# Performance work log

Measured on AMD Instinct MI355X. Metric: run time of the kernel, lower is better.

The kernel has to match this reference:

```python
import jax, jax.numpy as jnp
import numpy as np

DIM = 1536
RMS_EPS = 1e-7
LN_EPS = 1e-5


def rmsnorm(x, w):
    ms = jnp.mean(x * x, axis=-1, keepdims=True)
    return x / jnp.sqrt(ms + RMS_EPS) * w


def layernorm(x, w, b):
    mu = jnp.mean(x, axis=-1, keepdims=True)
    var = jnp.mean((x - mu) ** 2, axis=-1, keepdims=True)
    return (x - mu) / jnp.sqrt(var + LN_EPS) * w + b


def linear(x, W, b):
    # W stored as (in, out)
    return jnp.einsum('bnd,df->bnf', x, W) + b


def setup_inputs() -> dict:
    key = jax.random.key(0)
    ks = jax.random.split(key, 32)
    D = DIM
    s = 0.02
    inp = {
        'x': jax.random.normal(ks[0], (2, 4096, D), jnp.float32),
        'text_emb': jax.random.normal(ks[1], (2, 512, D), jnp.float32),
        # norm params
        'sq_w': jnp.ones((D,), jnp.float32),
        'sk_w': jnp.ones((D,), jnp.float32),
        'cq_w': jnp.ones((D,), jnp.float32),
        'ck_w': jnp.ones((D,), jnp.float32),
        'ln_w': jnp.ones((D,), jnp.float32),
        'ln_b': jnp.zeros((D,), jnp.float32),
        # self-attn projections
        'Wq': jax.random.normal(ks[2], (D, D), jnp.float32) * s,
        'bq': jnp.zeros((D,), jnp.float32),
        'Wk': jax.random.normal(ks[3], (D, D), jnp.float32) * s,
        'bk': jnp.zeros((D,), jnp.float32),
        'Wv': jax.random.normal(ks[4], (D, D), jnp.float32) * s,
        'bv': jnp.zeros((D,), jnp.float32),
        'Wo': jax.random.normal(ks[5], (D, D), jnp.float32) * s,
        'bo': jnp.zeros((D,), jnp.float32),
        # cross-attn projections
        'CWq': jax.random.normal(ks[6], (D, D), jnp.float32) * s,
        'Cbq': jnp.zeros((D,), jnp.float32),
        'CWk': jax.random.normal(ks[7], (D, D), jnp.float32) * s,
        'Cbk': jnp.zeros((D,), jnp.float32),
        'CWv': jax.random.normal(ks[8], (D, D), jnp.float32) * s,
        'Cbv': jnp.zeros((D,), jnp.float32),
        'CWo': jax.random.normal(ks[9], (D, D), jnp.float32) * s,
        'Cbo': jnp.zeros((D,), jnp.float32),
        # FFN
        'W1': jax.random.normal(ks[10], (D, 4 * D), jnp.float32) * s,
        'b1': jnp.zeros((4 * D,), jnp.float32),
        'W2': jax.random.normal(ks[11], (4 * D, D), jnp.float32) * s,
        'b2': jnp.zeros((D,), jnp.float32),
    }
    return inp


def reference(x, text_emb, sq_w, sk_w, cq_w, ck_w, ln_w, ln_b,
              Wq, bq, Wk, bk, Wv, bv, Wo, bo,
              CWq, Cbq, CWk, Cbk, CWv, Cbv, CWo, Cbo,
              W1, b1, W2, b2):
    scale = 1.0 / jnp.sqrt(jnp.float32(DIM))  # NOTE: full-dim scale, no head split (faithful)

    # self-attention (single-head over full dim)
    q = linear(rmsnorm(x, sq_w), Wq, bq)
    k = linear(rmsnorm(x, sk_w), Wk, bk)
    v = linear(x, Wv, bv)
    attn = jax.nn.softmax(jnp.einsum('bnd,bmd->bnm', q, k) * scale, axis=-1)
    attn_out = linear(jnp.einsum('bnm,bmd->bnd', attn, v), Wo, bo)

    # cross-attention
    cq = linear(rmsnorm(x, cq_w), CWq, Cbq)
    ck = linear(rmsnorm(text_emb, ck_w), CWk, Cbk)
    cv = linear(text_emb, CWv, Cbv)
    cattn = jax.nn.softmax(jnp.einsum('bnd,bmd->bnm', cq, ck) * scale, axis=-1)
    cross_out = linear(jnp.einsum('bnm,bmd->bnd', cattn, cv), CWo, Cbo)

    # FFN with exact GELU (torch nn.GELU default)
    h = linear(layernorm(x, ln_w, ln_b), W1, b1)
    ffn_out = linear(jax.nn.gelu(h, approximate=False), W2, b2)

    return x + attn_out + cross_out + ffn_out
```

## Files before the change

kernel.cpp:

```cpp
#include <hip/hip_runtime.h>
#include <hip/hip_bf16.h>
#include <cmath>

#define DD 1536
#define FF 6144

typedef __bf16 bf16_t;
typedef __bf16 bf16x8 __attribute__((ext_vector_type(8)));
typedef __bf16 bf16x4 __attribute__((ext_vector_type(4)));
typedef float  f32x4  __attribute__((ext_vector_type(4)));

#define VM6 asm volatile("s_waitcnt vmcnt(6)" ::: "memory")
#define VM0 asm volatile("s_waitcnt vmcnt(0)" ::: "memory")
#define LGKM0 do { asm volatile("s_waitcnt lgkmcnt(0)" :::); __builtin_amdgcn_sched_barrier(0); } while (0)
#define BAR __builtin_amdgcn_s_barrier()

__device__ __forceinline__ void async_load16(const bf16_t* g, bf16_t* l) {
  __builtin_amdgcn_global_load_lds(
      (const __attribute__((address_space(1))) void*)g,
      (__attribute__((address_space(3))) void*)l, 16, 0, 0);
}

__device__ __forceinline__ bf16x8 ds_read128(unsigned int addr) {
  bf16x8 r;
  asm volatile("ds_read_b128 %0, %1" : "=v"(r) : "v"(addr));
  return r;
}

__device__ __forceinline__ void xcd_remap(int& bx, int& by) {
  const int gx = gridDim.x, gy = gridDim.y;
  int wg = by * gx + bx;
  const int nwg = gx * gy;
  const int q = nwg >> 3, r = nwg & 7, xcd = wg & 7, o = wg >> 3;
  wg = (xcd < r ? xcd * (q + 1) : r * (q + 1) + (xcd - r) * q) + o;
  bx = wg % gx;
  by = wg / gx;
}

__global__ __launch_bounds__(256) void transpose_to_bf16(
    const float* __restrict__ W, bf16_t* __restrict__ Wt, int K, int N,
    const float* __restrict__ s, int ldt) {
  __shared__ float tile[32][33];
  const int tx = threadIdx.x, ty = threadIdx.y;
  const int n0 = blockIdx.x * 32, k0 = blockIdx.y * 32;
#pragma unroll
  for (int i = 0; i < 4; i++)
    tile[ty + 8 * i][tx] = W[(size_t)(k0 + ty + 8 * i) * N + n0 + tx];
  __syncthreads();
  const float sc = (s != nullptr) ? s[k0 + tx] : 1.f;
#pragma unroll
  for (int i = 0; i < 4; i++)
    Wt[(size_t)(n0 + ty + 8 * i) * ldt + k0 + tx] = (bf16_t)(tile[tx][ty + 8 * i] * sc);
}

__global__ __launch_bounds__(256) void bias_add2(
    const float* __restrict__ a, const float* __restrict__ b, float* __restrict__ o, int n) {
  const int i = blockIdx.x * 256 + threadIdx.x;
  if (i < n) o[i] = a[i] + b[i];
}

__device__ __forceinline__ void breduce1(float& a) {
#pragma unroll
  for (int off = 32; off; off >>= 1) a += __shfl_xor(a, off);
  __shared__ float sa[4];
  const int w = threadIdx.x >> 6, ln = threadIdx.x & 63;
  if (ln == 0) sa[w] = a;
  __syncthreads();
  a = (sa[0] + sa[1]) + (sa[2] + sa[3]);
  __syncthreads();
}

__device__ __forceinline__ void breduce2(float& a, float& b) {
#pragma unroll
  for (int off = 32; off; off >>= 1) {
    a += __shfl_xor(a, off);
    b += __shfl_xor(b, off);
  }
  __shared__ float sa[4], sb[4];
  const int w = threadIdx.x >> 6, ln = threadIdx.x & 63;
  if (ln == 0) { sa[w] = a; sb[w] = b; }
  __syncthreads();
  a = (sa[0] + sa[1]) + (sa[2] + sa[3]);
  b = (sb[0] + sb[1]) + (sb[2] + sb[3]);
  __syncthreads();
}

__global__ __launch_bounds__(256) void norm_x2(
    const float* __restrict__ x, bf16_t* __restrict__ xr, bf16_t* __restrict__ xb) {
  const int row = blockIdx.x, t = threadIdx.x;
  const float* p = x + (size_t)row * DD;
  f32x4 v0 = ((const f32x4*)p)[t];
  f32x4 v1 = 0.0f;
  if (t < 128) v1 = ((const f32x4*)p)[256 + t];
  float s2 = 0.f;
#pragma unroll
  for (int e = 0; e < 4; e++) s2 += v0[e] * v0[e];
  if (t < 128) {
#pragma unroll
    for (int e = 0; e < 4; e++) s2 += v1[e] * v1[e];
  }
  breduce1(s2);
  const float rq = rsqrtf(s2 * (1.f / DD) + 1e-7f);
  auto emit = [&](int ci, f32x4 v) {
    bf16x4 orr, ob;
#pragma unroll
    for (int e = 0; e < 4; e++) {
      orr[e] = (bf16_t)(v[e] * rq);
      ob[e] = (bf16_t)v[e];
    }
    const size_t o = (size_t)row * DD + ci * 4;
    *(bf16x4*)(xr + o) = orr;
    *(bf16x4*)(xb + o) = ob;
  };
  emit(t, v0);
  if (t < 128) emit(256 + t, v1);
}

__global__ __launch_bounds__(256) void norm_ln(
    const float* __restrict__ x, const float* __restrict__ w,
    const float* __restrict__ bb, bf16_t* __restrict__ o) {
  const int row = blockIdx.x, t = threadIdx.x;
  const float* p = x + (size_t)row * DD;
  f32x4 v0 = ((const f32x4*)p)[t];
  f32x4 v1 = 0.0f;
  if (t < 128) v1 = ((const f32x4*)p)[256 + t];
  float s = 0.f, s2 = 0.f;
#pragma unroll
  for (int e = 0; e < 4; e++) { s += v0[e]; s2 += v0[e] * v0[e]; }
  if (t < 128) {
#pragma unroll
    for (int e = 0; e < 4; e++) { s += v1[e]; s2 += v1[e] * v1[e]; }
  }
  breduce2(s, s2);
  const float mu = s * (1.f / DD);
  const float rln = rsqrtf(s2 * (1.f / DD) - mu * mu + 1e-5f);
  auto emit = [&](int ci, f32x4 v) {
    const int i0 = ci * 4;
    bf16x4 ov;
#pragma unroll
    for (int e = 0; e < 4; e++)
      ov[e] = (bf16_t)((v[e] - mu) * rln * w[i0 + e] + bb[i0 + e]);
    *(bf16x4*)(o + (size_t)row * DD + i0) = ov;
  };
  emit(t, v0);
  if (t < 128) emit(256 + t, v1);
}

__global__ __launch_bounds__(256) void norm_t2(
    const float* __restrict__ te, bf16_t* __restrict__ tb, bf16_t* __restrict__ tck) {
  const int row = blockIdx.x, t = threadIdx.x;
  const float* p = te + (size_t)row * DD;
  f32x4 v0 = ((const f32x4*)p)[t];
  f32x4 v1 = 0.0f;
  if (t < 128) v1 = ((const f32x4*)p)[256 + t];
  float s2 = 0.f;
#pragma unroll
  for (int e = 0; e < 4; e++) s2 += v0[e] * v0[e];
  if (t < 128) {
#pragma unroll
    for (int e = 0; e < 4; e++) s2 += v1[e] * v1[e];
  }
  breduce1(s2);
  const float rq = rsqrtf(s2 * (1.f / DD) + 1e-7f);
  auto emit = [&](int ci, f32x4 v) {
    bf16x4 ob, oc;
#pragma unroll
    for (int e = 0; e < 4; e++) {
      ob[e] = (bf16_t)v[e];
      oc[e] = (bf16_t)(v[e] * rq);
    }
    const size_t o = (size_t)row * DD + ci * 4;
    *(bf16x4*)(tb + o) = ob;
    *(bf16x4*)(tck + o) = oc;
  };
  emit(t, v0);
  if (t < 128) emit(256 + t, v1);
}

template <int NC>
__global__ __launch_bounds__(256) void softmax_bf16(bf16_t* __restrict__ S) {
  const int t = threadIdx.x;
  bf16_t* sr = S + (size_t)blockIdx.x * NC;
  constexpr int NV = (NC / 8 + 255) / 256;
  float v[NV][8];
  float mx = -3.4e38f;
#pragma unroll
  for (int i = 0; i < NV; i++) {
    const int idx = t + i * 256;
    if (idx * 8 < NC) {
      bf16x8 b = ((const bf16x8*)sr)[idx];
#pragma unroll
      for (int e = 0; e < 8; e++) {
        v[i][e] = (float)b[e];
        mx = fmaxf(mx, v[i][e]);
      }
    }
  }
#pragma unroll
  for (int off = 32; off; off >>= 1) mx = fmaxf(mx, __shfl_xor(mx, off));
  __shared__ float sm[4];
  const int w = t >> 6, ln = t & 63;
  if (ln == 0) sm[w] = mx;
  __syncthreads();
  mx = fmaxf(fmaxf(sm[0], sm[1]), fmaxf(sm[2], sm[3]));
  __syncthreads();
  float sum = 0.f;
#pragma unroll
  for (int i = 0; i < NV; i++) {
    const int idx = t + i * 256;
    if (idx * 8 < NC) {
#pragma unroll
      for (int e = 0; e < 8; e++) {
        v[i][e] = __expf(v[i][e] - mx);
        sum += v[i][e];
      }
    }
  }
#pragma unroll
  for (int off = 32; off; off >>= 1) sum += __shfl_xor(sum, off);
  __shared__ float ss[4];
  if (ln == 0) ss[w] = sum;
  __syncthreads();
  sum = (ss[0] + ss[1]) + (ss[2] + ss[3]);
  const float inv = 1.f / sum;
#pragma unroll
  for (int i = 0; i < NV; i++) {
    const int idx = t + i * 256;
    if (idx * 8 < NC) {
      bf16x8 o;
#pragma unroll
      for (int e = 0; e < 8; e++) o[e] = (bf16_t)(v[i][e] * inv);
      ((bf16x8*)sr)[idx] = o;
    }
  }
}

enum { EPI_BF16 = 0, EPI_F32_SCALE = 1, EPI_ADD_X = 2, EPI_ACC = 3, EPI_GELU = 4, EPI_TRANS = 5, EPI_BF16S = 6 };

template <int EPI>
__device__ __forceinline__ void epi_frag(
    f32x4 v, int r0, int c, const float* bias, void* Cout, const float* Xres,
    int ldc, float scale, int t_ld, int t_bshift, size_t t_bstride) {
  const float bv = (bias != nullptr) ? bias[c] : 0.f;
  if constexpr (EPI == EPI_BF16) {
    bf16_t* C = (bf16_t*)Cout;
#pragma unroll
    for (int r = 0; r < 4; r++) C[(size_t)(r0 + r) * ldc + c] = (bf16_t)(v[r] + bv);
  } else if constexpr (EPI == EPI_F32_SCALE) {
    float* C = (float*)Cout;
#pragma unroll
    for (int r = 0; r < 4; r++) C[(size_t)(r0 + r) * ldc + c] = v[r] * scale;
  } else if constexpr (EPI == EPI_BF16S) {
    bf16_t* C = (bf16_t*)Cout;
#pragma unroll
    for (int r = 0; r < 4; r++) C[(size_t)(r0 + r) * ldc + c] = (bf16_t)(v[r] * scale);
  } else if constexpr (EPI == EPI_ADD_X) {
    float* C = (float*)Cout;
#pragma unroll
    for (int r = 0; r < 4; r++) {
      const size_t ix = (size_t)(r0 + r) * ldc + c;
      C[ix] = Xres[ix] + v[r] + bv;
    }
  } else if constexpr (EPI == EPI_ACC) {
    float* C = (float*)Cout;
#pragma unroll
    for (int r = 0; r < 4; r++) {
      const size_t ix = (size_t)(r0 + r) * ldc + c;
      C[ix] += v[r] + bv;
    }
  } else if constexpr (EPI == EPI_GELU) {
    bf16_t* C = (bf16_t*)Cout;
#pragma unroll
    for (int r = 0; r < 4; r++) {
      const float h = v[r] + bv;
      C[(size_t)(r0 + r) * ldc + c] = (bf16_t)(0.5f * h * (1.f + erff(h * 0.70710678118654752f)));
    }
  } else {
    const int b = r0 >> t_bshift;
    const int n = r0 & ((1 << t_bshift) - 1);
    bf16_t* C = (bf16_t*)Cout + (size_t)b * t_bstride + (size_t)c * t_ld + n;
    bf16x4 o;
#pragma unroll
    for (int r = 0; r < 4; r++) o[r] = (bf16_t)(v[r] + bv);
    *(bf16x4*)C = o;
  }
}

template <int EPI>
__global__ __launch_bounds__(256) void gemm_bt(
    const bf16_t* __restrict__ A, const bf16_t* __restrict__ B,
    const float* __restrict__ bias, void* __restrict__ Cout,
    const float* __restrict__ Xres,
    int nK, int lda, int ldb, int ldc, float scale,
    int bsh, size_t bstr, int t_ld, int t_bshift, size_t t_bstride) {
  __shared__ __align__(16) bf16_t As[2][128 * 32];
  __shared__ __align__(16) bf16_t Bs[2][128 * 32];
  const int tid = threadIdx.x;
  int bx = blockIdx.x, by = blockIdx.y;
  xcd_remap(bx, by);
  const int m0 = by * 128, n0 = bx * 128;
  const int wave = tid >> 6, lane = tid & 63, l15 = lane & 15, hi = lane >> 4;
  const int wm = wave >> 1, wn = wave & 1;
  const int srow = tid >> 2, scol = (tid & 3) << 3;

  const bf16_t* Bb = bsh ? (B + (size_t)(m0 >> bsh) * bstr) : B;
  const bf16_t* ga = A + (size_t)(m0 + srow) * lda + scol;
  const bf16_t* gb = Bb + (size_t)(n0 + srow) * ldb + scol;
  const int lo = wave * 512;

  f32x4 acc[4][4];
#pragma unroll
  for (int i = 0; i < 4; i++)
#pragma unroll
    for (int j = 0; j < 4; j++) acc[i][j] = 0.0f;

  auto stage = [&](int buf, int kt) {
    const bf16_t* a = ga + (size_t)kt * 32;
    const bf16_t* b = gb + (size_t)kt * 32;
    async_load16(a, &As[buf][lo]);
    async_load16(a + (size_t)64 * lda, &As[buf][2048 + lo]);
    async_load16(b, &Bs[buf][lo]);
    async_load16(b + (size_t)64 * ldb, &Bs[buf][2048 + lo]);
  };

  auto compute = [&](int buf) {
    bf16x8 af[4], bg[4];
#pragma unroll
    for (int i = 0; i < 4; i++)
      af[i] = *(const bf16x8*)&As[buf][(wm * 64 + i * 16 + l15) * 32 + hi * 8];
#pragma unroll
    for (int j = 0; j < 4; j++)
      bg[j] = *(const bf16x8*)&Bs[buf][(wn * 64 + j * 16 + l15) * 32 + hi * 8];
#pragma unroll
    for (int i = 0; i < 4; i++)
#pragma unroll
      for (int j = 0; j < 4; j++)
        acc[i][j] = __builtin_amdgcn_mfma_f32_16x16x32_bf16(af[i], bg[j], acc[i][j], 0, 0, 0);
  };

  stage(0, 0);
  __syncthreads();
  for (int kt = 0; kt < nK; ++kt) {
    if (kt + 1 < nK) stage((kt + 1) & 1, kt + 1);
    compute(kt & 1);
    __syncthreads();
  }

#pragma unroll
  for (int i = 0; i < 4; i++) {
    const int r0 = m0 + wm * 64 + i * 16 + hi * 4;
#pragma unroll
    for (int j = 0; j < 4; j++) {
      const int c = n0 + wn * 64 + j * 16 + l15;
      epi_frag<EPI>(acc[i][j], r0, c, bias, Cout, Xres, ldc, scale, t_ld, t_bshift, t_bstride);
    }
  }
}

template <int EPI>
__global__ __launch_bounds__(512, 2) void gemm8(
    const bf16_t* __restrict__ A, const bf16_t* __restrict__ B,
    const float* __restrict__ bias, void* __restrict__ Cout,
    const float* __restrict__ Xres,
    int nT, int lda, int ldb, int ldc, float scale,
    int bsh, size_t bstr, int t_ld, int t_bshift, size_t t_bstride) {
  __shared__ __align__(16) bf16_t As[2][256 * 64];
  __shared__ __align__(16) bf16_t Bs[2][256 * 64];
  const int tid = threadIdx.x;
  int bx = blockIdx.x, by = blockIdx.y;
  xcd_remap(bx, by);
  const int m0 = by * 256, n0 = bx * 256;
  const int wave = tid >> 6, lane = tid & 63, l15 = lane & 15, hi = lane >> 4;
  const int wm = wave >> 2, wn = wave & 3;

  const int srow = tid >> 3;
  const int scol = ((tid & 7) ^ (srow & 7)) << 3;
  const bf16_t* Bb = bsh ? (B + (size_t)(m0 >> bsh) * bstr) : B;
  const bf16_t* gA = A + (size_t)(m0 + srow) * lda + scol;
  const bf16_t* gB = Bb + (size_t)(n0 + srow) * ldb + scol;
  const int ldst = wave * 512;

  f32x4 acc[8][4];
#pragma unroll
  for (int i = 0; i < 8; i++)
#pragma unroll
    for (int j = 0; j < 4; j++) acc[i][j] = 0.0f;

  auto stgA = [&](int t, int half) {
    if (t >= nT) return;
    const int buf = t & 1, r0 = half << 7;
    const size_t kof = (size_t)t * 64;
    async_load16(gA + (size_t)r0 * lda + kof, &As[buf][r0 * 64 + ldst]);
    async_load16(gA + (size_t)(r0 + 64) * lda + kof, &As[buf][(r0 + 64) * 64 + ldst]);
  };
  auto stgB = [&](int t, int half) {
    if (t >= nT) return;
    const int buf = t & 1, r0 = half << 7;
    const size_t kof = (size_t)t * 64;
    async_load16(gB + (size_t)r0 * ldb + kof, &Bs[buf][r0 * 64 + ldst]);
    async_load16(gB + (size_t)(r0 + 64) * ldb + kof, &Bs[buf][(r0 + 64) * 64 + ldst]);
  };

  bf16x8 af[4][2], bg[2][2][2];
  auto LDA = [&](int buf, int mh) {
#pragma unroll
    for (int i = 0; i < 4; i++) {
      const int r = wm * 128 + (mh * 4 + i) * 16 + l15;
      const int rx = r & 7;
#pragma unroll
      for (int ks = 0; ks < 2; ks++)
        af[i][ks] = ds_read128((unsigned int)(size_t)&As[buf][r * 64 + (((hi + 4 * ks) ^ rx) << 3)]);
    }
  };
  auto LDB = [&](int buf, int nh) {
#pragma unroll
    for (int j = 0; j < 2; j++) {
      const int r = wn * 64 + (nh * 2 + j) * 16 + l15;
      const int rx = r & 7;
#pragma unroll
      for (int ks = 0; ks < 2; ks++)
        bg[nh][j][ks] = ds_read128((unsigned int)(size_t)&Bs[buf][r * 64 + (((hi + 4 * ks) ^ rx) << 3)]);
    }
  };
  auto MM = [&](int mh, int nh) {
    __builtin_amdgcn_s_setprio(1);
#pragma unroll
    for (int i = 0; i < 4; i++)
#pragma unroll
      for (int j = 0; j < 2; j++)
#pragma unroll
        for (int ks = 0; ks < 2; ks++)
          acc[mh * 4 + i][nh * 2 + j] = __builtin_amdgcn_mfma_f32_16x16x32_bf16(
              af[i][ks], bg[nh][j][ks], acc[mh * 4 + i][nh * 2 + j], 0, 0, 0);
    __builtin_amdgcn_s_setprio(0);
  };

  stgB(0, 0); stgB(0, 1); stgA(0, 0); stgA(0, 1);
  stgB(1, 0); stgB(1, 1); stgA(1, 0);
  if (nT > 1) { VM6; } else { VM0; }
  BAR;

  for (int k = 0; k < nT; ++k) {
    const int buf = k & 1;
    stgA(k + 1, 1);
    LDA(buf, 0);
    LDB(buf, 0);
    BAR;
    LGKM0;
    MM(0, 0);
    BAR;
    LDB(buf, 1);
    BAR;
    LGKM0;
    MM(0, 1);
    BAR;
    stgB(k + 2, 0);
    LDA(buf, 1);
    BAR;
    LGKM0;
    MM(1, 0);
    BAR;
    stgB(k + 2, 1);
    stgA(k + 2, 0);
    if (k + 2 < nT) { VM6; } else { VM0; }
    BAR;
    MM(1, 1);
    BAR;
  }

#pragma unroll
  for (int fi = 0; fi < 8; fi++) {
    const int r0 = m0 + wm * 128 + fi * 16 + hi * 4;
#pragma unroll
    for (int fj = 0; fj < 4; fj++) {
      const int c = n0 + wn * 64 + fj * 16 + l15;
      epi_frag<EPI>(acc[fi][fj], r0, c, bias, Cout, Xres, ldc, scale, t_ld, t_bshift, t_bstride);
    }
  }
}

extern "C" void kernel_launch(void* const* d_in, const int* in_sizes, int n_in,
                              void* d_out, int out_size, void* d_ws, size_t ws_size,
                              hipStream_t stream) {
  (void)in_sizes; (void)n_in; (void)out_size; (void)ws_size;
  const float* x   = (const float*)d_in[0];
  const float* te  = (const float*)d_in[1];
  const float* sqw = (const float*)d_in[2];
  const float* skw = (const float*)d_in[3];
  const float* cqw = (const float*)d_in[4];
  const float* ckw = (const float*)d_in[5];
  const float* lnw = (const float*)d_in[6];
  const float* lnb = (const float*)d_in[7];
  const float* Wq = (const float*)d_in[8];  const float* bq = (const float*)d_in[9];
  const float* Wk = (const float*)d_in[10]; const float* bk = (const float*)d_in[11];
  const float* Wv = (const float*)d_in[12]; const float* bv = (const float*)d_in[13];
  const float* Wo = (const float*)d_in[14]; const float* bo = (const float*)d_in[15];
  const float* CWq = (const float*)d_in[16]; const float* Cbq = (const float*)d_in[17];
  const float* CWk = (const float*)d_in[18]; const float* Cbk = (const float*)d_in[19];
  const float* CWv = (const float*)d_in[20]; const float* Cbv = (const float*)d_in[21];
  const float* CWo = (const float*)d_in[22]; const float* Cbo = (const float*)d_in[23];
  const float* W1 = (const float*)d_in[24]; const float* b1 = (const float*)d_in[25];
  const float* W2 = (const float*)d_in[26]; const float* b2 = (const float*)d_in[27];
  float* out = (float*)d_out;

  bf16_t* ws = (bf16_t*)d_ws;
  bf16_t* R0 = ws;
  bf16_t* R1 = ws + 9437184;
  bf16_t* R2 = ws + 18874368;
  bf16_t* Tb  = ws + 31457280;
  bf16_t* Tck = ws + 33030144;
  bf16_t* R4 = ws + 34603008;
  bf16_t* R5 = ws + 59768832;
  bf16_t* R6 = ws + 72351744;
  bf16_t* S  = ws;
  float* biascat = (float*)(ws + 84934656);
  float* biasm   = (float*)(ws + 84940800);
  bf16_t* CK  = R0;
  bf16_t* CVt = R0 + 1572864;
  bf16_t* Sc  = R0 + 3145728;
  bf16_t* H   = R4;

  const dim3 blk(256), blk8(512), tb(32, 8);
  const float scl = 0.025515518153991442f;

  auto T = [&](const float* W, bf16_t* Wt, int K, int N, const float* s, int ldt) {
    transpose_to_bf16<<<dim3(N / 32, K / 32), tb, 0, stream>>>(W, Wt, K, N, s, ldt);
  };
  auto g8 = [](int M, int N) { return dim3(N / 256, M / 256); };
  auto g4 = [](int M, int N) { return dim3(N / 128, M / 128); };

  hipMemcpyAsync(biascat, bq, DD * sizeof(float), hipMemcpyDeviceToDevice, stream);
  hipMemcpyAsync(biascat + DD, bk, DD * sizeof(float), hipMemcpyDeviceToDevice, stream);
  bias_add2<<<6, blk, 0, stream>>>(bo, Cbo, biasm, DD);

  norm_x2<<<8192, blk, 0, stream>>>(x, R2 , R4 );

  T(Wv, R0, DD, DD, nullptr, DD);
  gemm8<EPI_TRANS><<<g8(8192, DD), blk8, 0, stream>>>(R4 , R0, bv, R5, nullptr,
      24, DD, DD, 0, 1.f, 0, 0, 4096, 12, (size_t)DD * 4096);

  T(Wq, R1, DD, DD, sqw, DD);
  T(Wk, R1 + 2359296, DD, DD, skw, DD);
  T(CWq, R1 + 4718592, DD, DD, cqw, DD);
  gemm8<EPI_BF16><<<g8(8192, 3072), blk8, 0, stream>>>(R2, R1, biascat, R4, nullptr,
      24, DD, DD, 3072, 1.f, 0, 0, 0, 0, 0);
  gemm8<EPI_BF16><<<g8(8192, DD), blk8, 0, stream>>>(R2, R1 + 4718592, Cbq, R6, nullptr,
      24, DD, DD, DD, 1.f, 0, 0, 0, 0, 0);

  gemm8<EPI_BF16S><<<g8(8192, 4096), blk8, 0, stream>>>(R4 , R4 + DD , nullptr, S, nullptr,
      24, 3072, 3072, 4096, scl, 12, (size_t)4096 * 3072, 0, 0, 0);
  softmax_bf16<4096><<<8192, blk, 0, stream>>>(S);
  gemm8<EPI_BF16><<<g8(8192, DD), blk8, 0, stream>>>(S, R5, nullptr, R4, nullptr,
      64, 4096, 4096, 3072, 1.f, 12, (size_t)DD * 4096, 0, 0, 0);

  norm_t2<<<1024, blk, 0, stream>>>(te, Tb, Tck);
  T(CWk, R1, DD, DD, ckw, DD);
  gemm_bt<EPI_BF16><<<g4(1024, DD), blk, 0, stream>>>(Tck, R1, Cbk, CK, nullptr,
      48, DD, DD, DD, 1.f, 0, 0, 0, 0, 0);
  T(CWv, R1 + 2359296, DD, DD, nullptr, DD);
  gemm_bt<EPI_TRANS><<<g4(1024, DD), blk, 0, stream>>>(Tb, R1 + 2359296, Cbv, CVt, nullptr,
      48, DD, DD, 0, 1.f, 0, 0, 512, 9, (size_t)DD * 512);
  gemm_bt<EPI_BF16S><<<g4(8192, 512), blk, 0, stream>>>(R6 , CK, nullptr, Sc, nullptr,
      48, DD, DD, 512, scl, 12, (size_t)512 * DD, 0, 0, 0);
  softmax_bf16<512><<<8192, blk, 0, stream>>>(Sc);
  gemm8<EPI_BF16><<<g8(8192, DD), blk8, 0, stream>>>(Sc, CVt, nullptr, R4 + 1536, nullptr,
      8, 512, 512, 3072, 1.f, 12, (size_t)DD * 512, 0, 0, 0);

  T(Wo, R1, DD, DD, nullptr, 3072);
  T(CWo, R1 + 1536, DD, DD, nullptr, 3072);
  gemm8<EPI_ADD_X><<<g8(8192, DD), blk8, 0, stream>>>(R4, R1, biasm, out, x,
      48, 3072, 3072, DD, 1.f, 0, 0, 0, 0, 0);

  norm_ln<<<8192, blk, 0, stream>>>(x, lnw, lnb, R2);
  T(W1, R0, DD, FF, nullptr, DD);
  gemm8<EPI_GELU><<<g8(8192, FF), blk8, 0, stream>>>(R2, R0, b1, H, nullptr,
      24, DD, DD, FF, 1.f, 0, 0, 0, 0, 0);
  T(W2, R1, FF, DD, nullptr, FF);
  gemm8<EPI_ACC><<<g8(8192, DD), blk8, 0, stream>>>(H, R1, b2, out, nullptr,
      96, FF, FF, DD, 1.f, 0, 0, 0, 0, 0);
}
```

Baseline: 1.213 ms.

## Double-buffer GEMM register fragments to overlap LDS reads with MFMA

Splits the A/B register fragments into two sets so the LDS reads for the next quadrant, and for the next k-tile's first quadrant, are issued before the current MFMA block runs. Full lgkmcnt(0) waits become partial waits (4, 8, 0), and several barriers are removed, so LDS latency can hide behind matrix math. The cost is more live VGPRs, which may lower occupancy or cause spills, and a tighter reliance on barrier ordering so the prefetch does not read a buffer being overwritten.

```diff
diff --git a/kernel.cpp b/kernel.cpp
--- a/kernel.cpp
+++ b/kernel.cpp
@@ -12,7 +12,10 @@
 
 #define VM6 asm volatile("s_waitcnt vmcnt(6)" ::: "memory")
 #define VM0 asm volatile("s_waitcnt vmcnt(0)" ::: "memory")
-#define LGKM0 do { asm volatile("s_waitcnt lgkmcnt(0)" :::); __builtin_amdgcn_sched_barrier(0); } while (0)
+#define SB  __builtin_amdgcn_sched_barrier(0)
+#define LGKM_0 do { asm volatile("s_waitcnt lgkmcnt(0)" :::); SB; } while (0)
+#define LGKM_4 do { asm volatile("s_waitcnt lgkmcnt(4)" :::); SB; } while (0)
+#define LGKM_8 do { asm volatile("s_waitcnt lgkmcnt(8)" :::); SB; } while (0)
 #define BAR __builtin_amdgcn_s_barrier()
 
 __device__ __forceinline__ void async_load16(const bf16_t* g, bf16_t* l) {
@@ -401,28 +404,28 @@
     async_load16(gB + (size_t)(r0 + 64) * ldb + kof, &Bs[buf][(r0 + 64) * 64 + ldst]);
   };
 
-  bf16x8 af[4][2], bg[2][2][2];
-  auto LDA = [&](int buf, int mh) {
+  bf16x8 af0[4][2], af1[4][2], bg0[2][2], bg1[2][2];
+  auto LDAf = [&](bf16x8 (&dst)[4][2], int buf, int mh) {
 #pragma unroll
     for (int i = 0; i < 4; i++) {
       const int r = wm * 128 + (mh * 4 + i) * 16 + l15;
       const int rx = r & 7;
 #pragma unroll
       for (int ks = 0; ks < 2; ks++)
-        af[i][ks] = ds_read128((unsigned int)(size_t)&As[buf][r * 64 + (((hi + 4 * ks) ^ rx) << 3)]);
-    }
-  };
-  auto LDB = [&](int buf, int nh) {
+        dst[i][ks] = ds_read128((unsigned int)(size_t)&As[buf][r * 64 + (((hi + 4 * ks) ^ rx) << 3)]);
+    }
+  };
+  auto LDBf = [&](bf16x8 (&dst)[2][2], int buf, int nh) {
 #pragma unroll
     for (int j = 0; j < 2; j++) {
       const int r = wn * 64 + (nh * 2 + j) * 16 + l15;
       const int rx = r & 7;
 #pragma unroll
       for (int ks = 0; ks < 2; ks++)
-        bg[nh][j][ks] = ds_read128((unsigned int)(size_t)&Bs[buf][r * 64 + (((hi + 4 * ks) ^ rx) << 3)]);
-    }
-  };
-  auto MM = [&](int mh, int nh) {
+        dst[j][ks] = ds_read128((unsigned int)(size_t)&Bs[buf][r * 64 + (((hi + 4 * ks) ^ rx) << 3)]);
+    }
+  };
+  auto MM = [&](bf16x8 (&a)[4][2], bf16x8 (&b)[2][2], int mh, int nh) {
     __builtin_amdgcn_s_setprio(1);
 #pragma unroll
     for (int i = 0; i < 4; i++)
@@ -431,7 +434,7 @@
 #pragma unroll
         for (int ks = 0; ks < 2; ks++)
           acc[mh * 4 + i][nh * 2 + j] = __builtin_amdgcn_mfma_f32_16x16x32_bf16(
-              af[i][ks], bg[nh][j][ks], acc[mh * 4 + i][nh * 2 + j], 0, 0, 0);
+              a[i][ks], b[j][ks], acc[mh * 4 + i][nh * 2 + j], 0, 0, 0);
     __builtin_amdgcn_s_setprio(0);
   };
 
@@ -439,32 +442,37 @@
   stgB(1, 0); stgB(1, 1); stgA(1, 0);
   if (nT > 1) { VM6; } else { VM0; }
   BAR;
+  LDAf(af0, 0, 0);
+  LDBf(bg0, 0, 0);
+  SB;
 
   for (int k = 0; k < nT; ++k) {
     const int buf = k & 1;
     stgA(k + 1, 1);
-    LDA(buf, 0);
-    LDB(buf, 0);
+    LDBf(bg1, buf, 1);
+    SB;
+    LGKM_4;
+    MM(af0, bg0, 0, 0);
     BAR;
-    LGKM0;
-    MM(0, 0);
-    BAR;
-    LDB(buf, 1);
-    BAR;
-    LGKM0;
-    MM(0, 1);
+    LDAf(af1, buf, 1);
+    SB;
+    LGKM_8;
+    MM(af0, bg1, 0, 1);
     BAR;
     stgB(k + 2, 0);
-    LDA(buf, 1);
-    BAR;
-    LGKM0;
-    MM(1, 0);
+    LGKM_0;
+    MM(af1, bg0, 1, 0);
     BAR;
     stgB(k + 2, 1);
     stgA(k + 2, 0);
     if (k + 2 < nT) { VM6; } else { VM0; }
     BAR;
-    MM(1, 1);
+    if (k + 1 < nT) {
+      LDAf(af0, buf ^ 1, 0);
+      LDBf(bg0, buf ^ 1, 0);
+    }
+    SB;
+    MM(af1, bg1, 1, 1);
     BAR;
   }
 
```

New measurement: 1.994 ms. +64.4%, slower.

## Fuse V, Q, K and cross-Q projections into one GEMM over RMS-normalized input

Applied to the files above, without the earlier changes.

Replaces three separate projection GEMMs (V from raw bf16 x, QK concatenated, and cross-Q) with a single N=6144 GEMM over the RMS-normalized input, using a new epilogue that routes column ranges to the V-transposed, QK and CQ buffers. V is recovered by multiplying the normalized-input product by the stored per-row RMS, so the norm kernel no longer writes a raw bf16 copy of x. This cuts kernel launches and A-operand reads and fills the GPU with one larger grid. In exchange, V now goes through an extra bf16 rounding of x/rms followed by rescaling, and the epilogue branches per column.

```diff
diff --git a/kernel.cpp b/kernel.cpp
--- a/kernel.cpp
+++ b/kernel.cpp
@@ -85,8 +85,8 @@
   __syncthreads();
 }
 
-__global__ __launch_bounds__(256) void norm_x2(
-    const float* __restrict__ x, bf16_t* __restrict__ xr, bf16_t* __restrict__ xb) {
+__global__ __launch_bounds__(256) void norm_x1(
+    const float* __restrict__ x, bf16_t* __restrict__ xr, float* __restrict__ rqinv) {
   const int row = blockIdx.x, t = threadIdx.x;
   const float* p = x + (size_t)row * DD;
   f32x4 v0 = ((const f32x4*)p)[t];
@@ -100,17 +100,14 @@
     for (int e = 0; e < 4; e++) s2 += v1[e] * v1[e];
   }
   breduce1(s2);
-  const float rq = rsqrtf(s2 * (1.f / DD) + 1e-7f);
+  const float ms = s2 * (1.f / DD) + 1e-7f;
+  const float rq = rsqrtf(ms);
+  if (t == 0) rqinv[row] = sqrtf(ms);
   auto emit = [&](int ci, f32x4 v) {
-    bf16x4 orr, ob;
-#pragma unroll
-    for (int e = 0; e < 4; e++) {
-      orr[e] = (bf16_t)(v[e] * rq);
-      ob[e] = (bf16_t)v[e];
-    }
-    const size_t o = (size_t)row * DD + ci * 4;
-    *(bf16x4*)(xr + o) = orr;
-    *(bf16x4*)(xb + o) = ob;
+    bf16x4 orr;
+#pragma unroll
+    for (int e = 0; e < 4; e++) orr[e] = (bf16_t)(v[e] * rq);
+    *(bf16x4*)(xr + (size_t)row * DD + ci * 4) = orr;
   };
   emit(t, v0);
   if (t < 128) emit(256 + t, v1);
@@ -235,7 +232,7 @@
   }
 }
 
-enum { EPI_BF16 = 0, EPI_F32_SCALE = 1, EPI_ADD_X = 2, EPI_ACC = 3, EPI_GELU = 4, EPI_TRANS = 5, EPI_BF16S = 6 };
+enum { EPI_BF16 = 0, EPI_F32_SCALE = 1, EPI_ADD_X = 2, EPI_ACC = 3, EPI_GELU = 4, EPI_TRANS = 5, EPI_BF16S = 6, EPI_PROJ3 = 7 };
 
 template <int EPI>
 __device__ __forceinline__ void epi_frag(
@@ -275,7 +272,7 @@
       const float h = v[r] + bv;
       C[(size_t)(r0 + r) * ldc + c] = (bf16_t)(0.5f * h * (1.f + erff(h * 0.70710678118654752f)));
     }
-  } else {
+  } else if constexpr (EPI == EPI_TRANS) {
     const int b = r0 >> t_bshift;
     const int n = r0 & ((1 << t_bshift) - 1);
     bf16_t* C = (bf16_t*)Cout + (size_t)b * t_bstride + (size_t)c * t_ld + n;
@@ -283,6 +280,23 @@
 #pragma unroll
     for (int r = 0; r < 4; r++) o[r] = (bf16_t)(v[r] + bv);
     *(bf16x4*)C = o;
+  } else {
+    bf16_t* base = (bf16_t*)Cout;
+    if (c < 1536) {
+      const int b = r0 >> 12, n = r0 & 4095;
+      bf16_t* C = base + 25165824 + (size_t)b * ((size_t)DD * 4096) + (size_t)c * 4096 + n;
+      bf16x4 o;
+#pragma unroll
+      for (int r = 0; r < 4; r++) o[r] = (bf16_t)(v[r] * Xres[r0 + r] + bv);
+      *(bf16x4*)C = o;
+    } else if (c < 4608) {
+#pragma unroll
+      for (int r = 0; r < 4; r++) base[(size_t)(r0 + r) * 3072 + (c - 1536)] = (bf16_t)(v[r] + bv);
+    } else {
+      bf16_t* C = base + 37748736;
+#pragma unroll
+      for (int r = 0; r < 4; r++) C[(size_t)(r0 + r) * 1536 + (c - 4608)] = (bf16_t)(v[r] + bv);
+    }
   }
 }
 
@@ -513,8 +527,9 @@
   bf16_t* R5 = ws + 59768832;
   bf16_t* R6 = ws + 72351744;
   bf16_t* S  = ws;
-  float* biascat = (float*)(ws + 84934656);
-  float* biasm   = (float*)(ws + 84940800);
+  float* bcat4 = (float*)(ws + 84934656);
+  float* biasm = (float*)(ws + 84946944);
+  float* rqinv = (float*)(ws + 84950016);
   bf16_t* CK  = R0;
   bf16_t* CVt = R0 + 1572864;
   bf16_t* Sc  = R0 + 3145728;
@@ -529,23 +544,20 @@
   auto g8 = [](int M, int N) { return dim3(N / 256, M / 256); };
   auto g4 = [](int M, int N) { return dim3(N / 128, M / 128); };
 
-  hipMemcpyAsync(biascat, bq, DD * sizeof(float), hipMemcpyDeviceToDevice, stream);
-  hipMemcpyAsync(biascat + DD, bk, DD * sizeof(float), hipMemcpyDeviceToDevice, stream);
+  hipMemcpyAsync(bcat4,        bv,  DD * sizeof(float), hipMemcpyDeviceToDevice, stream);
+  hipMemcpyAsync(bcat4 + DD,   bq,  DD * sizeof(float), hipMemcpyDeviceToDevice, stream);
+  hipMemcpyAsync(bcat4 + 2*DD, bk,  DD * sizeof(float), hipMemcpyDeviceToDevice, stream);
+  hipMemcpyAsync(bcat4 + 3*DD, Cbq, DD * sizeof(float), hipMemcpyDeviceToDevice, stream);
   bias_add2<<<6, blk, 0, stream>>>(bo, Cbo, biasm, DD);
 
-  norm_x2<<<8192, blk, 0, stream>>>(x, R2 , R4 );
-
-  T(Wv, R0, DD, DD, nullptr, DD);
-  gemm8<EPI_TRANS><<<g8(8192, DD), blk8, 0, stream>>>(R4 , R0, bv, R5, nullptr,
-      24, DD, DD, 0, 1.f, 0, 0, 4096, 12, (size_t)DD * 4096);
-
-  T(Wq, R1, DD, DD, sqw, DD);
-  T(Wk, R1 + 2359296, DD, DD, skw, DD);
-  T(CWq, R1 + 4718592, DD, DD, cqw, DD);
-  gemm8<EPI_BF16><<<g8(8192, 3072), blk8, 0, stream>>>(R2, R1, biascat, R4, nullptr,
+  norm_x1<<<8192, blk, 0, stream>>>(x, R2, rqinv);
+
+  T(Wv,  R0,               DD, DD, nullptr, DD);
+  T(Wq,  R0 + 2359296,     DD, DD, sqw,     DD);
+  T(Wk,  R0 + 4718592,     DD, DD, skw,     DD);
+  T(CWq, R0 + 7077888,     DD, DD, cqw,     DD);
+  gemm8<EPI_PROJ3><<<g8(8192, FF), blk8, 0, stream>>>(R2, R0, bcat4, R4, rqinv,
       24, DD, DD, 3072, 1.f, 0, 0, 0, 0, 0);
-  gemm8<EPI_BF16><<<g8(8192, DD), blk8, 0, stream>>>(R2, R1 + 4718592, Cbq, R6, nullptr,
-      24, DD, DD, DD, 1.f, 0, 0, 0, 0, 0);
 
   gemm8<EPI_BF16S><<<g8(8192, 4096), blk8, 0, stream>>>(R4 , R4 + DD , nullptr, S, nullptr,
       24, 3072, 3072, 4096, scl, 12, (size_t)4096 * 3072, 0, 0, 0);
```

Result: faster. 1.170 ms (-3.5%).
